# Optimization experiments

Measured on AMD Instinct MI355X. Metric: run time of the kernel, lower is better.

The kernel has to match this reference:

```python
import jax, jax.numpy as jnp
import numpy as np

D_MODEL = 1024
D_HEAD = 64
N_HEADS = D_MODEL // D_HEAD
MAX_SEQ = 2048
BATCH = 2
SEQ = 2048


def setup_inputs() -> dict:
    key = jax.random.key(0)
    ks = jax.random.split(key, 10)
    s = 1.0 / np.sqrt(D_MODEL)
    return {
        "x": jax.random.normal(ks[0], (BATCH, SEQ, D_MODEL), dtype=jnp.float32),
        "Wq": jax.random.normal(ks[1], (D_MODEL, D_MODEL), dtype=jnp.float32) * s,
        "bq": jax.random.normal(ks[2], (D_MODEL,), dtype=jnp.float32) * 0.01,
        "Wk": jax.random.normal(ks[3], (D_MODEL, D_MODEL), dtype=jnp.float32) * s,
        "bk": jax.random.normal(ks[4], (D_MODEL,), dtype=jnp.float32) * 0.01,
        "Wv": jax.random.normal(ks[5], (D_MODEL, D_MODEL), dtype=jnp.float32) * s,
        "bv": jax.random.normal(ks[6], (D_MODEL,), dtype=jnp.float32) * 0.01,
        "Er": jax.random.normal(ks[7], (MAX_SEQ, D_HEAD), dtype=jnp.float32),
        "Wo": jax.random.normal(ks[8], (D_MODEL, D_MODEL), dtype=jnp.float32) * s,
        "bo": jax.random.normal(ks[9], (D_MODEL,), dtype=jnp.float32) * 0.01,
    }


def _s_rel(q, Er):
    # q: [B,H,S,Dh]; use last S rows of Er (start = max_seq - seq)
    S = q.shape[2]
    Er_slice = Er[Er.shape[0] - S:, :]                  # [S, Dh]
    qE = jnp.einsum("bhsd,ld->bhsl", q, Er_slice)       # [B,H,S,S]
    padded = jnp.pad(qE, ((0, 0), (0, 0), (0, 0), (1, 0)))  # [B,H,S,S+1]
    B, H, S1, S2 = padded.shape
    padded = padded.reshape(B, H, S2, S1)               # skew trick
    return padded[:, :, 1:, :]                          # [B,H,S,S]


def reference(x, Wq, bq, Wk, bk, Wv, bv, Er, Wo, bo):
    B, S, _ = x.shape
    scale = 1.0 / np.sqrt(D_HEAD)
    # projections (torch Linear: x @ W.T + b)
    def proj(W, b):
        return (x @ W.T + b).reshape(B, S, N_HEADS, D_HEAD).transpose(0, 2, 1, 3)
    q = proj(Wq, bq)   # [B,H,S,Dh]
    k = proj(Wk, bk)
    v = proj(Wv, bv)
    qk = jnp.einsum("bhsd,bhtd->bhst", q, k)            # [B,H,S,S]
    logits = (qk + _s_rel(q, Er)) * scale
    causal = jnp.tril(jnp.ones((S, S), dtype=bool))
    masked = jnp.where(causal[None, None], logits, -1e9)
    attn = jax.nn.softmax(masked, axis=-1)
    out = jnp.einsum("bhst,bhtd->bhsd", attn, v)        # [B,H,S,Dh]
    out = out.transpose(0, 2, 1, 3).reshape(B, S, D_MODEL)
    return out @ Wo.T + bo
```

## Files before the change

### kernel.cpp

```cpp
#include <hip/hip_runtime.h>
#include <hip/hip_bf16.h>

typedef short v8s __attribute__((ext_vector_type(8)));
typedef float v4f __attribute__((ext_vector_type(4)));
typedef __hip_bfloat16 bf16;
typedef unsigned int u32;

#define MFMA(a, b, c) __builtin_amdgcn_mfma_f32_16x16x32_bf16(a, b, c, 0, 0, 0)

__device__ __forceinline__ void gload16(const bf16* g, bf16* l) {
    __builtin_amdgcn_global_load_lds(
        (const __attribute__((address_space(1))) u32*)(g),
        (__attribute__((address_space(3))) u32*)(l), 16, 0, 0);
}

__global__ __launch_bounds__(256) void cast_all(
    const float* __restrict__ x,  const float* __restrict__ wq,
    const float* __restrict__ wk, const float* __restrict__ wv,
    const float* __restrict__ wo, const float* __restrict__ er,
    bf16* __restrict__ xb,  bf16* __restrict__ wqb, bf16* __restrict__ wkb,
    bf16* __restrict__ wvb, bf16* __restrict__ wob, bf16* __restrict__ erb)
{
    const int r = blockIdx.y;
    const float* s; bf16* d; int n4;
    if      (r == 0) { s = x;  d = xb;  n4 = 1048576; }
    else if (r == 1) { s = wq; d = wqb; n4 = 262144;  }
    else if (r == 2) { s = wk; d = wkb; n4 = 262144;  }
    else if (r == 3) { s = wv; d = wvb; n4 = 262144;  }
    else if (r == 4) { s = wo; d = wob; n4 = 262144;  }
    else             { s = er; d = erb; n4 = 32768;   }
    const int i = blockIdx.x * 256 + threadIdx.x;
    if (i < n4) {
        const float4 v = ((const float4*)s)[i];
        bf16 t[4];
        t[0] = __float2bfloat16(v.x);
        t[1] = __float2bfloat16(v.y);
        t[2] = __float2bfloat16(v.z);
        t[3] = __float2bfloat16(v.w);
        ((uint2*)d)[i] = *(const uint2*)t;
    }
}

__global__ __launch_bounds__(256) void gemm_nt(
    const bf16* __restrict__ A, const bf16* __restrict__ W,
    const float* __restrict__ b0, const float* __restrict__ b1,
    const float* __restrict__ b2,
    bf16* __restrict__ oHM, float* __restrict__ outf)
{
    __shared__ bf16 As[128 * 64];
    __shared__ bf16 Bs[128 * 64];

    const int tid = threadIdx.x;
    const int w  = tid >> 6, l = tid & 63;
    const int lm = l & 15,  lq = l >> 4;
    const int wm = (w >> 1) * 64, wn = (w & 1) * 64;
    const int m0 = blockIdx.y * 128, n0 = blockIdx.x * 128;

    const int grow = l >> 3;
    const int gcol = ((l & 7) ^ grow) * 8;

    v4f acc[4][4];
#pragma unroll
    for (int i = 0; i < 4; ++i)
#pragma unroll
        for (int j = 0; j < 4; ++j) acc[i][j] = (v4f){0.f, 0.f, 0.f, 0.f};

    const int sw = (lm & 7) << 4;

    for (int k0 = 0; k0 < 1024; k0 += 64) {
        __syncthreads();
#pragma unroll
        for (int q = 0; q < 4; ++q) {
            const int rr = w * 32 + q * 8;
            gload16(&A[(size_t)(m0 + rr + grow) * 1024 + k0 + gcol], &As[rr * 64]);
            gload16(&W[(size_t)(n0 + rr + grow) * 1024 + k0 + gcol], &Bs[rr * 64]);
        }
        __syncthreads();
#pragma unroll
        for (int kk = 0; kk < 2; ++kk) {
            v8s a[4], b[4];
            const int cb = (lq * 16 + kk * 64);
#pragma unroll
            for (int i = 0; i < 4; ++i) {
                const int row = wm + i * 16 + lm;
                a[i] = *(const v8s*)((const char*)As + row * 128 + (cb ^ sw));
            }
#pragma unroll
            for (int j = 0; j < 4; ++j) {
                const int row = wn + j * 16 + lm;
                b[j] = *(const v8s*)((const char*)Bs + row * 128 + (cb ^ sw));
            }
#pragma unroll
            for (int i = 0; i < 4; ++i)
#pragma unroll
                for (int j = 0; j < 4; ++j)
                    acc[i][j] = MFMA(a[i], b[j], acc[i][j]);
        }
    }

    const int z = blockIdx.x >> 3;
    const float* bias = (z == 0) ? b0 : (z == 1) ? b1 : b2;

    float bv[4];
#pragma unroll
    for (int j = 0; j < 4; ++j) bv[j] = bias[(n0 & 1023) + wn + j * 16 + lm];

#pragma unroll
    for (int i = 0; i < 4; ++i) {
#pragma unroll
        for (int j = 0; j < 4; ++j) {
            const int col = n0 + wn + j * 16 + lm;
            const int cc  = col & 1023;
#pragma unroll
            for (int r = 0; r < 4; ++r) {
                const int row = m0 + wm + i * 16 + lq * 4 + r;
                const float v = acc[i][j][r] + bv[j];
                if (outf) {
                    outf[(size_t)row * 1024 + cc] = v;
                } else {
                    const int bb = row >> 11, ss = row & 2047;
                    const int hh = cc >> 6,  dd = cc & 63;
                    oHM[(size_t)z * 4194304 +
                        ((size_t)(bb * 16 + hh) * 2048 + ss) * 64 + dd] = __float2bfloat16(v);
                }
            }
        }
    }
}

__global__ __launch_bounds__(256) void vtrans(const bf16* __restrict__ V, bf16* __restrict__ Vt)
{
    __shared__ bf16 T[64 * 72];
    const int s0  = blockIdx.x * 64;
    const int bh  = blockIdx.y;
    const int tid = threadIdx.x;
#pragma unroll
    for (int rep = 0; rep < 2; ++rep) {
        const int unit = tid + rep * 256;
        const int sl = unit >> 3, d8 = (unit & 7) * 8;
        *(uint4*)&T[sl * 72 + d8] = *(const uint4*)&V[((size_t)bh * 2048 + s0 + sl) * 64 + d8];
    }
    __syncthreads();
#pragma unroll
    for (int rep = 0; rep < 2; ++rep) {
        const int unit = tid + rep * 256;
        const int d = unit >> 3, t8 = (unit & 7) * 8;
        unsigned short tmp[8];
#pragma unroll
        for (int j = 0; j < 8; ++j) tmp[j] = *(const unsigned short*)&T[(t8 + j) * 72 + d];
        *(uint4*)&Vt[((size_t)bh * 64 + d) * 2048 + s0 + t8] = *(const uint4*)tmp;
    }
}

__global__ __launch_bounds__(256, 4) void attn(
    const bf16* __restrict__ Q, const bf16* __restrict__ K,
    const bf16* __restrict__ Vt, const bf16* __restrict__ Er,
    bf16* __restrict__ AO)
{
    __shared__ bf16 Ks[64 * 72];
    __shared__ bf16 Vs[64 * 72];
    __shared__ bf16 Ps[64 * 72];
    __shared__ bf16 Gs[64 * 84];

    const int ord = blockIdx.x;
    const int u = ord & 255, j = ord >> 8;
    const int a = u & 31, yh = u >> 5;
    const int q1 = (j & 2) ? (a ^ 16) : a;
    const int qb = (j & 1) ? (31 - q1) : q1;
    const int bh = 8 * j + yh;

    const int i0 = qb * 64;
    const int b  = bh >> 4, h = bh & 15;
    const int tid = threadIdx.x;
    const int w  = tid >> 6, l = tid & 63;
    const int lm = l & 15,  lq = l >> 4;

    const bf16* qp = Q + ((size_t)bh * 2048 + i0 + w * 16 + lm) * 64 + lq * 8;
    const v8s q0 = *(const v8s*)qp;
    const v8s q1f = *(const v8s*)(qp + 32);

    v4f accO[4];
#pragma unroll
    for (int dt = 0; dt < 4; ++dt) accO[dt] = (v4f){0.f, 0.f, 0.f, 0.f};
    float rs[4];
#pragma unroll
    for (int r = 0; r < 4; ++r) rs[r] = 0.f;

    const int sr0 = tid >> 3;
    const int sc8 = (tid & 7) * 8;
    const size_t kbase = (size_t)bh * 2048 * 64;
    const size_t vbase = (size_t)bh * 64 * 2048;

    const int nk = qb + 1;

    uint4 kp0 = *(const uint4*)&K[kbase + (size_t)sr0 * 64 + sc8];
    uint4 kp1 = *(const uint4*)&K[kbase + (size_t)(sr0 + 32) * 64 + sc8];
    uint4 vp0 = *(const uint4*)&Vt[vbase + (size_t)sr0 * 2048 + sc8];
    uint4 vp1 = *(const uint4*)&Vt[vbase + (size_t)(sr0 + 32) * 2048 + sc8];

    for (int it = 0; it < nk; ++it) {
        const int j0 = it * 64;
        __syncthreads();
        *(uint4*)&Ks[sr0 * 72 + sc8]        = kp0;
        *(uint4*)&Ks[(sr0 + 32) * 72 + sc8] = kp1;
        *(uint4*)&Vs[sr0 * 72 + sc8]        = vp0;
        *(uint4*)&Vs[(sr0 + 32) * 72 + sc8] = vp1;
        if (it + 1 < nk) {
            const int jn = j0 + 64;
            kp0 = *(const uint4*)&K[kbase + (size_t)(jn + sr0) * 64 + sc8];
            kp1 = *(const uint4*)&K[kbase + (size_t)(jn + sr0 + 32) * 64 + sc8];
            vp0 = *(const uint4*)&Vt[vbase + (size_t)sr0 * 2048 + jn + sc8];
            vp1 = *(const uint4*)&Vt[vbase + (size_t)(sr0 + 32) * 2048 + jn + sc8];
        }
        const int basew = 2048 - 16 - i0 + j0 - 16 * w;
#pragma unroll
        for (int ct2 = 0; ct2 < 5; ++ct2) {
            int mr = basew + ct2 * 16 + lm;
            mr = (mr > 2047) ? 2047 : mr;
            const bf16* ep = Er + (size_t)mr * 64 + lq * 8;
            const v8s e0 = *(const v8s*)ep;
            const v8s e1 = *(const v8s*)(ep + 32);
            v4f g = (v4f){0.f, 0.f, 0.f, 0.f};
            g = MFMA(q0, e0, g);
            g = MFMA(q1f, e1, g);
#pragma unroll
            for (int r = 0; r < 4; ++r)
                Gs[(w * 16 + lq * 4 + r) * 84 + ct2 * 16 + lm] =
                    __float2bfloat16(g[r] * 0.125f);
        }
        __syncthreads();
        v4f sv[4];
#pragma unroll
        for (int ct = 0; ct < 4; ++ct) {
            const v8s k0f = *(const v8s*)&Ks[(ct * 16 + lm) * 72 + lq * 8];
            const v8s k1f = *(const v8s*)&Ks[(ct * 16 + lm) * 72 + 32 + lq * 8];
            v4f s = (v4f){0.f, 0.f, 0.f, 0.f};
            s = MFMA(q0, k0f, s);
            s = MFMA(q1f, k1f, s);
            sv[ct] = s;
        }
#pragma unroll
        for (int r = 0; r < 4; ++r) {
            const int rl = lq * 4 + r;
            const int ig = i0 + w * 16 + rl;
#pragma unroll
            for (int ct = 0; ct < 4; ++ct) {
                const int jj = ct * 16 + lm;
                const float gb = (float)Gs[(w * 16 + rl) * 84 + jj + 15 - rl];
                float s = fmaf(sv[ct][r], 0.125f, gb);
                if (j0 + jj > ig) s = -1e9f;
                const float pe = __expf(s - 4.0f);
                rs[r] += pe;
                Ps[(w * 16 + rl) * 72 + jj] = __float2bfloat16(pe);
            }
        }
        const v8s pa0 = *(const v8s*)&Ps[(w * 16 + lm) * 72 + lq * 8];
        const v8s pa1 = *(const v8s*)&Ps[(w * 16 + lm) * 72 + 32 + lq * 8];
#pragma unroll
        for (int dt = 0; dt < 4; ++dt) {
            const v8s vb0 = *(const v8s*)&Vs[(dt * 16 + lm) * 72 + lq * 8];
            const v8s vb1 = *(const v8s*)&Vs[(dt * 16 + lm) * 72 + 32 + lq * 8];
            accO[dt] = MFMA(pa0, vb0, accO[dt]);
            accO[dt] = MFMA(pa1, vb1, accO[dt]);
        }
    }
#pragma unroll
    for (int r = 0; r < 4; ++r) {
#pragma unroll
        for (int msk = 8; msk >= 1; msk >>= 1)
            rs[r] += __shfl_xor(rs[r], msk, 64);
    }
#pragma unroll
    for (int dt = 0; dt < 4; ++dt) {
#pragma unroll
        for (int r = 0; r < 4; ++r) {
            const int row = i0 + w * 16 + lq * 4 + r;
            const int d   = dt * 16 + lm;
            const float v = accO[dt][r] / rs[r];
            AO[((size_t)b * 2048 + row) * 1024 + h * 64 + d] = __float2bfloat16(v);
        }
    }
}

extern "C" void kernel_launch(void* const* d_in, const int* in_sizes, int n_in,
                              void* d_out, int out_size, void* d_ws, size_t ws_size,
                              hipStream_t stream)
{
    const float* x  = (const float*)d_in[0];
    const float* Wq = (const float*)d_in[1];
    const float* bq = (const float*)d_in[2];
    const float* Wk = (const float*)d_in[3];
    const float* bk = (const float*)d_in[4];
    const float* Wv = (const float*)d_in[5];
    const float* bv = (const float*)d_in[6];
    const float* Er = (const float*)d_in[7];
    const float* Wo = (const float*)d_in[8];
    const float* bo = (const float*)d_in[9];
    float* out = (float*)d_out;

    bf16* ws = (bf16*)d_ws;
    const size_t NEl = (size_t)4096 * 1024;
    bf16* Qw  = ws;
    bf16* Kw  = ws + NEl;
    bf16* Vw  = ws + 2 * NEl;
    bf16* Vtw = ws + 3 * NEl;
    bf16* xb  = ws + 4 * NEl;
    bf16* AOw = xb;
    bf16* Wqb = ws + 5 * NEl;
    bf16* Wkb = Wqb + 1024 * 1024;
    bf16* Wvb = Wkb + 1024 * 1024;
    bf16* Wob = Wvb + 1024 * 1024;
    bf16* Erb = Wob + 1024 * 1024;
    (void)Kw; (void)Vw; (void)Wkb; (void)Wvb;

    cast_all<<<dim3(4096, 6), 256, 0, stream>>>(x, Wq, Wk, Wv, Wo, Er,
                                                xb, Wqb, Wkb, Wvb, Wob, Erb);
    gemm_nt<<<dim3(24, 32), 256, 0, stream>>>(xb, Wqb, bq, bk, bv, Qw, nullptr);
    vtrans<<<dim3(32, 32), 256, 0, stream>>>(Vw, Vtw);
    attn<<<dim3(1024), 256, 0, stream>>>(Qw, Kw, Vtw, Erb, AOw);
    gemm_nt<<<dim3(8, 32), 256, 0, stream>>>(AOw, Wob, bo, bo, bo, nullptr, out);
}
```

Measured before the change: 278.3 us.

## Fuse V transpose into QKV GEMM epilogue and vectorize output stores

Swaps the MFMA operand order so each lane holds four consecutive output columns, which lets the GEMM and attention epilogues write packed 8/16-byte stores instead of scalar ones. The V projection now writes directly in transposed layout from the GEMM epilogue, which removes the separate vtrans kernel launch and its extra read/write pass over V. The attention epilogue shuffles the row sums to match the transposed accumulator layout and multiplies by a reciprocal instead of dividing. The Vt writes are strided 2-byte scatters, which may coalesce poorly.

New measurement: 287.0 us. 3.1% more time.

```diff
diff --git a/kernel.cpp b/kernel.cpp
--- a/kernel.cpp
+++ b/kernel.cpp
@@ -45,7 +45,7 @@
     const bf16* __restrict__ A, const bf16* __restrict__ W,
     const float* __restrict__ b0, const float* __restrict__ b1,
     const float* __restrict__ b2,
-    bf16* __restrict__ oHM, float* __restrict__ outf)
+    bf16* __restrict__ oHM, bf16* __restrict__ Vt, float* __restrict__ outf)
 {
     __shared__ bf16 As[128 * 64];
     __shared__ bf16 Bs[128 * 64];
@@ -94,61 +94,49 @@
             for (int i = 0; i < 4; ++i)
 #pragma unroll
                 for (int j = 0; j < 4; ++j)
-                    acc[i][j] = MFMA(a[i], b[j], acc[i][j]);
+                    acc[i][j] = MFMA(b[j], a[i], acc[i][j]);
         }
     }
 
     const int z = blockIdx.x >> 3;
     const float* bias = (z == 0) ? b0 : (z == 1) ? b1 : b2;
 
-    float bv[4];
-#pragma unroll
-    for (int j = 0; j < 4; ++j) bv[j] = bias[(n0 & 1023) + wn + j * 16 + lm];
+    float4 bj[4];
+#pragma unroll
+    for (int j = 0; j < 4; ++j)
+        bj[j] = *(const float4*)&bias[(n0 & 1023) + wn + j * 16 + lq * 4];
 
 #pragma unroll
     for (int i = 0; i < 4; ++i) {
+        const int row = m0 + wm + i * 16 + lm;
+        const int bb = row >> 11, ss = row & 2047;
 #pragma unroll
         for (int j = 0; j < 4; ++j) {
-            const int col = n0 + wn + j * 16 + lm;
-            const int cc  = col & 1023;
-#pragma unroll
-            for (int r = 0; r < 4; ++r) {
-                const int row = m0 + wm + i * 16 + lq * 4 + r;
-                const float v = acc[i][j][r] + bv[j];
-                if (outf) {
-                    outf[(size_t)row * 1024 + cc] = v;
+            const int cc = (n0 & 1023) + wn + j * 16 + lq * 4;
+            const float v0 = acc[i][j][0] + bj[j].x;
+            const float v1 = acc[i][j][1] + bj[j].y;
+            const float v2 = acc[i][j][2] + bj[j].z;
+            const float v3 = acc[i][j][3] + bj[j].w;
+            if (outf) {
+                const float4 fv = {v0, v1, v2, v3};
+                *(float4*)&outf[(size_t)row * 1024 + cc] = fv;
+            } else {
+                bf16 t[4];
+                t[0] = __float2bfloat16(v0);
+                t[1] = __float2bfloat16(v1);
+                t[2] = __float2bfloat16(v2);
+                t[3] = __float2bfloat16(v3);
+                const int hh = cc >> 6, dd = cc & 63;
+                if (z < 2) {
+                    *(uint2*)&oHM[(size_t)z * 4194304 +
+                        ((size_t)(bb * 16 + hh) * 2048 + ss) * 64 + dd] = *(uint2*)t;
                 } else {
-                    const int bb = row >> 11, ss = row & 2047;
-                    const int hh = cc >> 6,  dd = cc & 63;
-                    oHM[(size_t)z * 4194304 +
-                        ((size_t)(bb * 16 + hh) * 2048 + ss) * 64 + dd] = __float2bfloat16(v);
+#pragma unroll
+                    for (int r = 0; r < 4; ++r)
+                        Vt[((size_t)(bb * 16 + hh) * 64 + dd + r) * 2048 + ss] = t[r];
                 }
             }
         }
-    }
-}
-
-__global__ __launch_bounds__(256) void vtrans(const bf16* __restrict__ V, bf16* __restrict__ Vt)
-{
-    __shared__ bf16 T[64 * 72];
-    const int s0  = blockIdx.x * 64;
-    const int bh  = blockIdx.y;
-    const int tid = threadIdx.x;
-#pragma unroll
-    for (int rep = 0; rep < 2; ++rep) {
-        const int unit = tid + rep * 256;
-        const int sl = unit >> 3, d8 = (unit & 7) * 8;
-        *(uint4*)&T[sl * 72 + d8] = *(const uint4*)&V[((size_t)bh * 2048 + s0 + sl) * 64 + d8];
-    }
-    __syncthreads();
-#pragma unroll
-    for (int rep = 0; rep < 2; ++rep) {
-        const int unit = tid + rep * 256;
-        const int d = unit >> 3, t8 = (unit & 7) * 8;
-        unsigned short tmp[8];
-#pragma unroll
-        for (int j = 0; j < 8; ++j) tmp[j] = *(const unsigned short*)&T[(t8 + j) * 72 + d];
-        *(uint4*)&Vt[((size_t)bh * 64 + d) * 2048 + s0 + t8] = *(const uint4*)tmp;
     }
 }
 
@@ -260,8 +248,8 @@
         for (int dt = 0; dt < 4; ++dt) {
             const v8s vb0 = *(const v8s*)&Vs[(dt * 16 + lm) * 72 + lq * 8];
             const v8s vb1 = *(const v8s*)&Vs[(dt * 16 + lm) * 72 + 32 + lq * 8];
-            accO[dt] = MFMA(pa0, vb0, accO[dt]);
-            accO[dt] = MFMA(pa1, vb1, accO[dt]);
+            accO[dt] = MFMA(vb0, pa0, accO[dt]);
+            accO[dt] = MFMA(vb1, pa1, accO[dt]);
         }
     }
 #pragma unroll
@@ -270,15 +258,21 @@
         for (int msk = 8; msk >= 1; msk >>= 1)
             rs[r] += __shfl_xor(rs[r], msk, 64);
     }
+    const int srcl = (lm >> 2) * 16;
+    const float s0 = __shfl(rs[0], srcl, 64);
+    const float s1 = __shfl(rs[1], srcl, 64);
+    const float s2 = __shfl(rs[2], srcl, 64);
+    const float s3 = __shfl(rs[3], srcl, 64);
+    const float den = (lm & 2) ? ((lm & 1) ? s3 : s2) : ((lm & 1) ? s1 : s0);
+    const float inv = 1.0f / den;
+    const int rowo = i0 + w * 16 + lm;
 #pragma unroll
     for (int dt = 0; dt < 4; ++dt) {
-#pragma unroll
-        for (int r = 0; r < 4; ++r) {
-            const int row = i0 + w * 16 + lq * 4 + r;
-            const int d   = dt * 16 + lm;
-            const float v = accO[dt][r] / rs[r];
-            AO[((size_t)b * 2048 + row) * 1024 + h * 64 + d] = __float2bfloat16(v);
-        }
+        bf16 t[4];
+#pragma unroll
+        for (int r = 0; r < 4; ++r) t[r] = __float2bfloat16(accO[dt][r] * inv);
+        *(uint2*)&AO[((size_t)b * 2048 + rowo) * 1024 + h * 64 + dt * 16 + lq * 4] =
+            *(uint2*)t;
     }
 }
 
@@ -302,7 +296,6 @@
     const size_t NEl = (size_t)4096 * 1024;
     bf16* Qw  = ws;
     bf16* Kw  = ws + NEl;
-    bf16* Vw  = ws + 2 * NEl;
     bf16* Vtw = ws + 3 * NEl;
     bf16* xb  = ws + 4 * NEl;
     bf16* AOw = xb;
@@ -311,12 +304,11 @@
     bf16* Wvb = Wkb + 1024 * 1024;
     bf16* Wob = Wvb + 1024 * 1024;
     bf16* Erb = Wob + 1024 * 1024;
-    (void)Kw; (void)Vw; (void)Wkb; (void)Wvb;
+    (void)Kw;
 
     cast_all<<<dim3(4096, 6), 256, 0, stream>>>(x, Wq, Wk, Wv, Wo, Er,
                                                 xb, Wqb, Wkb, Wvb, Wob, Erb);
-    gemm_nt<<<dim3(24, 32), 256, 0, stream>>>(xb, Wqb, bq, bk, bv, Qw, nullptr);
-    vtrans<<<dim3(32, 32), 256, 0, stream>>>(Vw, Vtw);
+    gemm_nt<<<dim3(24, 32), 256, 0, stream>>>(xb, Wqb, bq, bk, bv, Qw, Vtw, nullptr);
     attn<<<dim3(1024), 256, 0, stream>>>(Qw, Kw, Vtw, Erb, AOw);
-    gemm_nt<<<dim3(8, 32), 256, 0, stream>>>(AOw, Wob, bo, bo, bo, nullptr, out);
-}
+    gemm_nt<<<dim3(8, 32), 256, 0, stream>>>(AOw, Wob, bo, bo, bo, nullptr, nullptr, out);
+}
```
